# Kernel optimization log

Hardware: AMD Instinct MI355X
Metric: run time of the kernel (lower is better)

## Reference

```python
import jax, jax.numpy as jnp
import numpy as np

N, DEG, D_COORD, D_CH, D_HID = 20000, 32, 3, 64, 256
E = N * DEG


def setup_inputs() -> dict:
    key = jax.random.key(0)
    ks = jax.random.split(key, 12)
    y = jax.random.normal(ks[0], (N, D_COORD), dtype=jnp.float32)
    x = jax.random.normal(ks[1], (N, D_COORD), dtype=jnp.float32)
    f_y = jax.random.normal(ks[2], (N, D_CH), dtype=jnp.float32)
    # quadrature weights ~ 1/|A(x)| scale
    weights = jax.random.uniform(ks[3], (N,), dtype=jnp.float32) / DEG
    neighbors_index = jax.random.randint(ks[4], (E,), 0, N, dtype=jnp.int32)
    neighbors_row_splits = (jnp.arange(N + 1, dtype=jnp.int32) * DEG)
    d_in = 2 * D_COORD + D_CH  # 70: concat(y_nbr, x_self, f_nbr) for 'nonlinear'
    W1 = jax.random.normal(ks[5], (d_in, D_HID), dtype=jnp.float32) / np.sqrt(d_in)
    b1 = jnp.zeros((D_HID,), dtype=jnp.float32)
    W2 = jax.random.normal(ks[6], (D_HID, D_HID), dtype=jnp.float32) / np.sqrt(D_HID)
    b2 = jnp.zeros((D_HID,), dtype=jnp.float32)
    W3 = jax.random.normal(ks[7], (D_HID, D_CH), dtype=jnp.float32) / np.sqrt(D_HID)
    b3 = jnp.zeros((D_CH,), dtype=jnp.float32)
    return {"y": y, "x": x, "f_y": f_y, "weights": weights,
            "neighbors_index": neighbors_index,
            "neighbors_row_splits": neighbors_row_splits,
            "W1": W1, "b1": b1, "W2": W2, "b2": b2, "W3": W3, "b3": b3}


def reference(y, x, f_y, weights, neighbors_index, neighbors_row_splits,
              W1, b1, W2, b2, W3, b3):
    n = y.shape[0]
    e = neighbors_index.shape[0]
    # CSR -> per-edge segment id (equivalent to torch repeat_interleave(num_reps))
    seg = jnp.searchsorted(neighbors_row_splits, jnp.arange(e), side='right') - 1
    rep_features = y[neighbors_index]      # [E, d1] gathered neighbor coords
    self_features = x[seg]                 # [E, d2] repeated query coords
    in_features = f_y[neighbors_index]     # [E, d3] gathered function values
    # transform_type == 'nonlinear': kernel sees (x, y, f(y))
    agg = jnp.concatenate([rep_features, self_features, in_features], axis=-1)
    h = jax.nn.gelu(agg @ W1 + b1, approximate=False)
    h = jax.nn.gelu(h @ W2 + b2, approximate=False)
    k = h @ W3 + b3                        # [E, d3]
    # (d): k(x,y,f(y)) * f(y), then weighted segment-CSR sum
    msg = weights[neighbors_index][:, None] * (k * in_features)
    out = jax.ops.segment_sum(msg, seg, num_segments=n)  # [n, d3]
    return out[None]  # [1, n, d3] (batch of 1)
```

## Files before the change

kernel.cpp:

```cpp
#include <hip/hip_runtime.h>
#include <math.h>
#include <stdint.h>

#define NN   20000
#define DEG  32
#define DIN  70
#define KP   96
#define DH   256
#define DC   64
#define NT   512
#define ET   64
#define NPB  2

typedef _Float16 f16;
typedef _Float16 f16x4 __attribute__((ext_vector_type(4)));
typedef _Float16 f16x8 __attribute__((ext_vector_type(8)));
typedef float    f32x4 __attribute__((ext_vector_type(4)));

#define AGG_P 104
#define YF_P  72

#define W1T_OFF 0
#define W2T_OFF (256*KP)
#define W3T_OFF (256*KP + 256*DH)
#define YF_OFF  (256*KP + 256*DH + DC*DH)

__device__ __forceinline__ float gelu_fast(float v) {
    float u  = v * 0.70710678118654752f;
    float a  = fabsf(u);
    float t  = __builtin_amdgcn_rcpf(fmaf(0.3275911f, a, 1.0f));
    float p  = fmaf(1.061405429f, t, -1.453152027f);
    p = fmaf(p, t, 1.421413741f);
    p = fmaf(p, t, -0.284496736f);
    p = fmaf(p, t, 0.254829592f);
    p = p * t;
    float e  = __expf(-u * u);
    float er = fmaf(-p, e, 1.0f);
    er = copysignf(er, u);
    return 0.5f * v * (1.0f + er);
}

__device__ __forceinline__ f16* h_at(f16* base, int row, int col) {
    uint32_t off = (uint32_t)(row << 9) + ((uint32_t)(col << 1) ^ (uint32_t)((row & 7) << 4));
    return (f16*)((char*)base + off);
}

__global__ void prep_weights(const float* __restrict__ W1,
                             const float* __restrict__ W2,
                             const float* __restrict__ W3,
                             f16* __restrict__ ws)
{
    int t = blockIdx.x * blockDim.x + threadIdx.x;
    if (t < W2T_OFF) {
        int n = t / KP, k = t - n * KP;
        float v;
        if (k < 3)              v = W1[(3 + k) * DH + n];
        else if (k < 8)         v = 0.0f;
        else if (k < 72)        v = W1[(6 + (k - 8)) * DH + n];
        else if (k < 75)        v = W1[(k - 72) * DH + n];
        else                    v = 0.0f;
        ws[t] = (f16)v;
    } else if (t < W3T_OFF) {
        int u = t - W2T_OFF;
        int n = u >> 8, k = u & 255;
        ws[t] = (f16)W2[k * DH + n];
    } else if (t < W3T_OFF + DC * DH) {
        int u = t - W3T_OFF;
        int n = u >> 8, k = u & 255;
        ws[t] = (f16)W3[k * DC + n];
    }
}

__global__ void prep_yf(const float* __restrict__ y,
                        const float* __restrict__ f_y,
                        f16* __restrict__ yf)
{
    int idx = blockIdx.x * blockDim.x + threadIdx.x;
    if (idx >= NN * YF_P) return;
    int n = idx / YF_P, c = idx - n * YF_P;
    float v;
    if (c < DC)          v = f_y[n * DC + c];
    else if (c < DC + 3) v = y[n * 3 + (c - DC)];
    else                 v = 0.0f;
    yf[idx] = (f16)v;
}

__global__ __launch_bounds__(NT, 6)
void it_mfma_kernel(const float* __restrict__ x,
                    const float* __restrict__ wq,
                    const int*   __restrict__ nbr,
                    const float* __restrict__ b1,
                    const float* __restrict__ b2,
                    const float* __restrict__ b3,
                    const f16*  __restrict__ ws,
                    float* __restrict__ out)
{
    const int blk  = blockIdx.x;
    const int t    = threadIdx.x;
    const int lane = t & 63;
    const int w    = t >> 6;
    const int l15  = lane & 15;
    const int lk   = lane >> 4;

    const f16* w1t = ws + W1T_OFF;
    const f16* w2t = ws + W2T_OFF;
    const f16* w3t = ws + W3T_OFF;
    const f16* yf  = ws + YF_OFF;

    __shared__ __align__(16) unsigned char s_u[ET * DH * 2];
    f16 (*s_agg)[AGG_P] = (f16(*)[AGG_P])s_u;
    f16* s_h0 = (f16*)s_u;
    __shared__ int   s_nbr[ET];
    __shared__ float s_wq[ET];
    __shared__ float s_red[4][DC];

    if (t < ET) {
        int n = nbr[blk * ET + t];
        s_nbr[t] = n;
        s_wq[t]  = wq[n];
    }
    __syncthreads();

    {
        const int e    = t >> 3;
        const int part = t & 7;
        const f16* yfr = yf + (size_t)s_nbr[e] * YF_P;
        f16* aggr = &s_agg[e][0];
        #pragma unroll
        for (int j = 0; j < 2; ++j) {
            int ch = part + j * 8;
            if (ch == 0) {
                int node = blk * NPB + (e >> 5);
                f16x8 v = {};
                v[0] = (f16)x[node*3 + 0];
                v[1] = (f16)x[node*3 + 1];
                v[2] = (f16)x[node*3 + 2];
                *(f16x8*)&aggr[0] = v;
            } else if (ch <= 9) {
                *(f16x8*)&aggr[8*ch] = *(const f16x8*)&yfr[8*(ch-1)];
            } else if (ch < 12) {
                *(f16x8*)&aggr[8*ch] = (f16x8){};
            }
        }
    }
    __syncthreads();

    const int n_base = w * 32;

    f32x4 acc[4][2];

    #pragma unroll
    for (int nj = 0; nj < 2; ++nj) {
        float4 bv = *(const float4*)&b1[n_base + nj*16 + lk*4];
        #pragma unroll
        for (int mi = 0; mi < 4; ++mi) acc[mi][nj] = (f32x4){bv.x, bv.y, bv.z, bv.w};
    }
    #pragma unroll
    for (int ks = 0; ks < KP/32; ++ks) {
        const int k0 = ks*32 + lk*8;
        f16x8 a0 = *(const f16x8*)&s_agg[ 0 + l15][k0];
        f16x8 a1 = *(const f16x8*)&s_agg[16 + l15][k0];
        f16x8 a2 = *(const f16x8*)&s_agg[32 + l15][k0];
        f16x8 a3 = *(const f16x8*)&s_agg[48 + l15][k0];
        #pragma unroll
        for (int nj = 0; nj < 2; ++nj) {
            f16x8 b = *(const f16x8*)&w1t[(n_base + nj*16 + l15) * KP + k0];
            acc[0][nj] = __builtin_amdgcn_mfma_f32_16x16x32_f16(b, a0, acc[0][nj], 0, 0, 0);
            acc[1][nj] = __builtin_amdgcn_mfma_f32_16x16x32_f16(b, a1, acc[1][nj], 0, 0, 0);
            acc[2][nj] = __builtin_amdgcn_mfma_f32_16x16x32_f16(b, a2, acc[2][nj], 0, 0, 0);
            acc[3][nj] = __builtin_amdgcn_mfma_f32_16x16x32_f16(b, a3, acc[3][nj], 0, 0, 0);
        }
    }
    __syncthreads();
    #pragma unroll
    for (int mi = 0; mi < 4; ++mi)
        #pragma unroll
        for (int nj = 0; nj < 2; ++nj) {
            int e  = mi*16 + l15;
            int n0 = n_base + nj*16 + lk*4;
            f16x4 hv;
            #pragma unroll
            for (int r = 0; r < 4; ++r) hv[r] = (f16)gelu_fast(acc[mi][nj][r]);
            *(f16x4*)h_at(s_h0, e, n0) = hv;
        }
    __syncthreads();

    #pragma unroll
    for (int nj = 0; nj < 2; ++nj) {
        float4 bv = *(const float4*)&b2[n_base + nj*16 + lk*4];
        #pragma unroll
        for (int mi = 0; mi < 4; ++mi) acc[mi][nj] = (f32x4){bv.x, bv.y, bv.z, bv.w};
    }
    #pragma unroll 2
    for (int ks = 0; ks < DH/32; ++ks) {
        const int k0 = ks*32 + lk*8;
        f16x8 a0 = *(const f16x8*)h_at(s_h0,  0 + l15, k0);
        f16x8 a1 = *(const f16x8*)h_at(s_h0, 16 + l15, k0);
        f16x8 a2 = *(const f16x8*)h_at(s_h0, 32 + l15, k0);
        f16x8 a3 = *(const f16x8*)h_at(s_h0, 48 + l15, k0);
        #pragma unroll
        for (int nj = 0; nj < 2; ++nj) {
            f16x8 b = *(const f16x8*)&w2t[(n_base + nj*16 + l15) * DH + k0];
            acc[0][nj] = __builtin_amdgcn_mfma_f32_16x16x32_f16(b, a0, acc[0][nj], 0, 0, 0);
            acc[1][nj] = __builtin_amdgcn_mfma_f32_16x16x32_f16(b, a1, acc[1][nj], 0, 0, 0);
            acc[2][nj] = __builtin_amdgcn_mfma_f32_16x16x32_f16(b, a2, acc[2][nj], 0, 0, 0);
            acc[3][nj] = __builtin_amdgcn_mfma_f32_16x16x32_f16(b, a3, acc[3][nj], 0, 0, 0);
        }
    }
    __syncthreads();
    #pragma unroll
    for (int mi = 0; mi < 4; ++mi)
        #pragma unroll
        for (int nj = 0; nj < 2; ++nj) {
            int e  = mi*16 + l15;
            int n0 = n_base + nj*16 + lk*4;
            f16x4 hv;
            #pragma unroll
            for (int r = 0; r < 4; ++r) hv[r] = (f16)gelu_fast(acc[mi][nj][r]);
            *(f16x4*)h_at(s_h0, e, n0) = hv;
        }
    __syncthreads();

    {
        const int g       = w & 3;
        const int ch_base = (w >> 2) * 32;
        f32x4 acc3[2];
        #pragma unroll
        for (int nj = 0; nj < 2; ++nj) {
            float4 bv = *(const float4*)&b3[ch_base + nj*16 + lk*4];
            acc3[nj] = (f32x4){bv.x, bv.y, bv.z, bv.w};
        }
        #pragma unroll 2
        for (int ks = 0; ks < DH/32; ++ks) {
            const int k0 = ks*32 + lk*8;
            f16x8 h = *(const f16x8*)h_at(s_h0, g*16 + l15, k0);
            #pragma unroll
            for (int nj = 0; nj < 2; ++nj) {
                f16x8 wf = *(const f16x8*)&w3t[(ch_base + nj*16 + l15) * DH + k0];
                acc3[nj] = __builtin_amdgcn_mfma_f32_16x16x32_f16(wf, h, acc3[nj], 0, 0, 0);
            }
        }
        const int e = g*16 + l15;
        const f16* yfr = yf + (size_t)s_nbr[e] * YF_P;
        const float wqe = s_wq[e];
        #pragma unroll
        for (int nj = 0; nj < 2; ++nj) {
            f16x4 fq = *(const f16x4*)&yfr[ch_base + nj*16 + lk*4];
            f32x4 p;
            #pragma unroll
            for (int r = 0; r < 4; ++r)
                p[r] = wqe * acc3[nj][r] * (float)fq[r];
            #pragma unroll
            for (int m = 1; m <= 8; m <<= 1) {
                #pragma unroll
                for (int r = 0; r < 4; ++r)
                    p[r] += __shfl_xor(p[r], m, 64);
            }
            if (l15 == 0)
                *(f32x4*)&s_red[g][ch_base + nj*16 + lk*4] = p;
        }
    }
    __syncthreads();

    if (t < NPB * DC) {
        int node = t >> 6, c = t & 63;
        out[(blk * NPB + node) * DC + c] = s_red[2*node][c] + s_red[2*node + 1][c];
    }
}

extern "C" void kernel_launch(void* const* d_in, const int* in_sizes, int n_in,
                              void* d_out, int out_size, void* d_ws, size_t ws_size,
                              hipStream_t stream) {
    const float* y   = (const float*)d_in[0];
    const float* x   = (const float*)d_in[1];
    const float* f_y = (const float*)d_in[2];
    const float* wq  = (const float*)d_in[3];
    const int*   nbr = (const int*)d_in[4];
    const float* W1  = (const float*)d_in[6];
    const float* b1  = (const float*)d_in[7];
    const float* W2  = (const float*)d_in[8];
    const float* b2  = (const float*)d_in[9];
    const float* W3  = (const float*)d_in[10];
    const float* b3  = (const float*)d_in[11];
    float* out = (float*)d_out;
    f16*   ws  = (f16*)d_ws;

    hipLaunchKernelGGL(prep_weights, dim3((W3T_OFF + DC*DH + 255) / 256), dim3(256), 0, stream,
                       W1, W2, W3, ws);
    hipLaunchKernelGGL(prep_yf, dim3((NN * YF_P + 255) / 256), dim3(256), 0, stream,
                       y, f_y, ws + YF_OFF);
    hipLaunchKernelGGL(it_mfma_kernel, dim3(NN / NPB), dim3(NT), 0, stream,
                       x, wq, nbr, b1, b2, b3, ws, out);
}
```

Baseline: 375.5 us.

## Split LDS buffers, swizzle h layout, prefetch weights, reuse gathered features

Gives the activation buffer its own LDS region instead of aliasing it with the aggregated-input buffer. Layer-1 output can then be written without the barrier that kept layer-1 reads from overlapping it, and layer-3 reads f(y) from LDS instead of re-gathering it from global memory. Weight fragments are now prefetched one k-step ahead, and LDS addresses use precomputed swizzled offsets. The cost is more LDS per block (about 13 KB extra), which may lower occupancy against the 6-block launch bound. The shared neighbor-index staging is also dropped, so each thread reloads nbr and wq from global memory.

```diff
diff --git a/kernel.cpp b/kernel.cpp
--- a/kernel.cpp
+++ b/kernel.cpp
@@ -4,7 +4,6 @@
 
 #define NN   20000
 #define DEG  32
-#define DIN  70
 #define KP   96
 #define DH   256
 #define DC   64
@@ -38,11 +37,6 @@
     float er = fmaf(-p, e, 1.0f);
     er = copysignf(er, u);
     return 0.5f * v * (1.0f + er);
-}
-
-__device__ __forceinline__ f16* h_at(f16* base, int row, int col) {
-    uint32_t off = (uint32_t)(row << 9) + ((uint32_t)(col << 1) ^ (uint32_t)((row & 7) << 4));
-    return (f16*)((char*)base + off);
 }
 
 __global__ void prep_weights(const float* __restrict__ W1,
@@ -89,9 +83,9 @@
 void it_mfma_kernel(const float* __restrict__ x,
                     const float* __restrict__ wq,
                     const int*   __restrict__ nbr,
-                    const float* __restrict__ b1,
-                    const float* __restrict__ b2,
-                    const float* __restrict__ b3,
+                    const float* __restrict__ bias1,
+                    const float* __restrict__ bias2,
+                    const float* __restrict__ bias3,
                     const f16*  __restrict__ ws,
                     float* __restrict__ out)
 {
@@ -101,30 +95,24 @@
     const int w    = t >> 6;
     const int l15  = lane & 15;
     const int lk   = lane >> 4;
+    const int mm   = l15 & 7;
+    const int mlo  = mm & 3, mhi = mm >> 2;
 
     const f16* w1t = ws + W1T_OFF;
     const f16* w2t = ws + W2T_OFF;
     const f16* w3t = ws + W3T_OFF;
     const f16* yf  = ws + YF_OFF;
 
-    __shared__ __align__(16) unsigned char s_u[ET * DH * 2];
-    f16 (*s_agg)[AGG_P] = (f16(*)[AGG_P])s_u;
-    f16* s_h0 = (f16*)s_u;
-    __shared__ int   s_nbr[ET];
-    __shared__ float s_wq[ET];
+    __shared__ __align__(16) f16 s_agg[ET][AGG_P];
+    __shared__ __align__(16) f16 s_h[ET * DH];
     __shared__ float s_red[4][DC];
-
-    if (t < ET) {
-        int n = nbr[blk * ET + t];
-        s_nbr[t] = n;
-        s_wq[t]  = wq[n];
-    }
-    __syncthreads();
+    f16* s_h0 = s_h;
 
     {
         const int e    = t >> 3;
         const int part = t & 7;
-        const f16* yfr = yf + (size_t)s_nbr[e] * YF_P;
+        const int n    = nbr[blk * ET + e];
+        const f16* yfr = yf + (size_t)n * YF_P;
         f16* aggr = &s_agg[e][0];
         #pragma unroll
         for (int j = 0; j < 2; ++j) {
@@ -147,114 +135,165 @@
 
     const int n_base = w * 32;
 
+    uint32_t rbE[4], rbO[4];
+    #pragma unroll
+    for (int mi = 0; mi < 4; ++mi) {
+        rbE[mi] = (uint32_t)((mi*16 + l15) << 9) + (uint32_t)(mhi << 6)
+                + (uint32_t)((lk ^ mlo) << 4);
+        rbO[mi] = rbE[mi] ^ 64u;
+    }
+    const uint32_t wb = (uint32_t)(l15 << 9) + (uint32_t)((w >> 1) << 7)
+                      + (uint32_t)(((w & 1) ^ mhi) << 6)
+                      + (uint32_t)(((mm >> 1) & 1) << 5)
+                      + (uint32_t)((lk << 3) ^ ((mm & 1) << 4));
+    char* wp0 = (char*)s_h0 + wb;
+    char* wp1 = (char*)s_h0 + (wb ^ 32u);
+
     f32x4 acc[4][2];
+
+    {
+        const f16* w1r0 = &w1t[(n_base + l15) * KP];
+        const f16* w1r1 = &w1t[(n_base + 16 + l15) * KP];
+        f16x8 wf0[3], wf1[3];
+        #pragma unroll
+        for (int ks = 0; ks < 3; ++ks) {
+            wf0[ks] = *(const f16x8*)&w1r0[ks*32 + lk*8];
+            wf1[ks] = *(const f16x8*)&w1r1[ks*32 + lk*8];
+        }
+        #pragma unroll
+        for (int nj = 0; nj < 2; ++nj) {
+            float4 bv = *(const float4*)&bias1[n_base + nj*16 + lk*4];
+            #pragma unroll
+            for (int mi = 0; mi < 4; ++mi) acc[mi][nj] = (f32x4){bv.x, bv.y, bv.z, bv.w};
+        }
+        #pragma unroll
+        for (int ks = 0; ks < 3; ++ks) {
+            f16x8 a0 = *(const f16x8*)&s_agg[ 0 + l15][ks*32 + lk*8];
+            f16x8 a1 = *(const f16x8*)&s_agg[16 + l15][ks*32 + lk*8];
+            f16x8 a2 = *(const f16x8*)&s_agg[32 + l15][ks*32 + lk*8];
+            f16x8 a3 = *(const f16x8*)&s_agg[48 + l15][ks*32 + lk*8];
+            acc[0][0] = __builtin_amdgcn_mfma_f32_16x16x32_f16(wf0[ks], a0, acc[0][0], 0, 0, 0);
+            acc[0][1] = __builtin_amdgcn_mfma_f32_16x16x32_f16(wf1[ks], a0, acc[0][1], 0, 0, 0);
+            acc[1][0] = __builtin_amdgcn_mfma_f32_16x16x32_f16(wf0[ks], a1, acc[1][0], 0, 0, 0);
+            acc[1][1] = __builtin_amdgcn_mfma_f32_16x16x32_f16(wf1[ks], a1, acc[1][1], 0, 0, 0);
+            acc[2][0] = __builtin_amdgcn_mfma_f32_16x16x32_f16(wf0[ks], a2, acc[2][0], 0, 0, 0);
+            acc[2][1] = __builtin_amdgcn_mfma_f32_16x16x32_f16(wf1[ks], a2, acc[2][1], 0, 0, 0);
+            acc[3][0] = __builtin_amdgcn_mfma_f32_16x16x32_f16(wf0[ks], a3, acc[3][0], 0, 0, 0);
+            acc[3][1] = __builtin_amdgcn_mfma_f32_16x16x32_f16(wf1[ks], a3, acc[3][1], 0, 0, 0);
+        }
+    }
+    #pragma unroll
+    for (int mi = 0; mi < 4; ++mi) {
+        #pragma unroll
+        for (int nj = 0; nj < 2; ++nj) {
+            f16x4 hv;
+            #pragma unroll
+            for (int r = 0; r < 4; ++r) hv[r] = (f16)gelu_fast(acc[mi][nj][r]);
+            *(f16x4*)((nj ? wp1 : wp0) + mi*8192) = hv;
+        }
+    }
+    __syncthreads();
 
     #pragma unroll
     for (int nj = 0; nj < 2; ++nj) {
-        float4 bv = *(const float4*)&b1[n_base + nj*16 + lk*4];
+        float4 bv = *(const float4*)&bias2[n_base + nj*16 + lk*4];
         #pragma unroll
         for (int mi = 0; mi < 4; ++mi) acc[mi][nj] = (f32x4){bv.x, bv.y, bv.z, bv.w};
     }
+    {
+        const f16* w2r0 = &w2t[(n_base + l15) * DH];
+        const f16* w2r1 = &w2t[(n_base + 16 + l15) * DH];
+        f16x8 bc0 = *(const f16x8*)&w2r0[lk*8];
+        f16x8 bc1 = *(const f16x8*)&w2r1[lk*8];
+        #pragma unroll
+        for (int ks = 0; ks < 8; ++ks) {
+            f16x8 bn0, bn1;
+            if (ks < 7) {
+                bn0 = *(const f16x8*)&w2r0[(ks+1)*32 + lk*8];
+                bn1 = *(const f16x8*)&w2r1[(ks+1)*32 + lk*8];
+            }
+            const uint32_t ro = (uint32_t)(ks >> 1) * 128u;
+            f16x8 a0, a1, a2, a3;
+            if (ks & 1) {
+                a0 = *(const f16x8*)((char*)s_h0 + rbO[0] + ro);
+                a1 = *(const f16x8*)((char*)s_h0 + rbO[1] + ro);
+                a2 = *(const f16x8*)((char*)s_h0 + rbO[2] + ro);
+                a3 = *(const f16x8*)((char*)s_h0 + rbO[3] + ro);
+            } else {
+                a0 = *(const f16x8*)((char*)s_h0 + rbE[0] + ro);
+                a1 = *(const f16x8*)((char*)s_h0 + rbE[1] + ro);
+                a2 = *(const f16x8*)((char*)s_h0 + rbE[2] + ro);
+                a3 = *(const f16x8*)((char*)s_h0 + rbE[3] + ro);
+            }
+            acc[0][0] = __builtin_amdgcn_mfma_f32_16x16x32_f16(bc0, a0, acc[0][0], 0, 0, 0);
+            acc[0][1] = __builtin_amdgcn_mfma_f32_16x16x32_f16(bc1, a0, acc[0][1], 0, 0, 0);
+            acc[1][0] = __builtin_amdgcn_mfma_f32_16x16x32_f16(bc0, a1, acc[1][0], 0, 0, 0);
+            acc[1][1] = __builtin_amdgcn_mfma_f32_16x16x32_f16(bc1, a1, acc[1][1], 0, 0, 0);
+            acc[2][0] = __builtin_amdgcn_mfma_f32_16x16x32_f16(bc0, a2, acc[2][0], 0, 0, 0);
+            acc[2][1] = __builtin_amdgcn_mfma_f32_16x16x32_f16(bc1, a2, acc[2][1], 0, 0, 0);
+            acc[3][0] = __builtin_amdgcn_mfma_f32_16x16x32_f16(bc0, a3, acc[3][0], 0, 0, 0);
+            acc[3][1] = __builtin_amdgcn_mfma_f32_16x16x32_f16(bc1, a3, acc[3][1], 0, 0, 0);
+            bc0 = bn0; bc1 = bn1;
+        }
+    }
+    __syncthreads();
     #pragma unroll
-    for (int ks = 0; ks < KP/32; ++ks) {
-        const int k0 = ks*32 + lk*8;
-        f16x8 a0 = *(const f16x8*)&s_agg[ 0 + l15][k0];
-        f16x8 a1 = *(const f16x8*)&s_agg[16 + l15][k0];
-        f16x8 a2 = *(const f16x8*)&s_agg[32 + l15][k0];
-        f16x8 a3 = *(const f16x8*)&s_agg[48 + l15][k0];
-        #pragma unroll
-        for (int nj = 0; nj < 2; ++nj) {
-            f16x8 b = *(const f16x8*)&w1t[(n_base + nj*16 + l15) * KP + k0];
-            acc[0][nj] = __builtin_amdgcn_mfma_f32_16x16x32_f16(b, a0, acc[0][nj], 0, 0, 0);
-            acc[1][nj] = __builtin_amdgcn_mfma_f32_16x16x32_f16(b, a1, acc[1][nj], 0, 0, 0);
-            acc[2][nj] = __builtin_amdgcn_mfma_f32_16x16x32_f16(b, a2, acc[2][nj], 0, 0, 0);
-            acc[3][nj] = __builtin_amdgcn_mfma_f32_16x16x32_f16(b, a3, acc[3][nj], 0, 0, 0);
-        }
-    }
-    __syncthreads();
-    #pragma unroll
-    for (int mi = 0; mi < 4; ++mi)
-        #pragma unroll
-        for (int nj = 0; nj < 2; ++nj) {
-            int e  = mi*16 + l15;
-            int n0 = n_base + nj*16 + lk*4;
+    for (int mi = 0; mi < 4; ++mi) {
+        #pragma unroll
+        for (int nj = 0; nj < 2; ++nj) {
             f16x4 hv;
             #pragma unroll
             for (int r = 0; r < 4; ++r) hv[r] = (f16)gelu_fast(acc[mi][nj][r]);
-            *(f16x4*)h_at(s_h0, e, n0) = hv;
-        }
-    __syncthreads();
-
-    #pragma unroll
-    for (int nj = 0; nj < 2; ++nj) {
-        float4 bv = *(const float4*)&b2[n_base + nj*16 + lk*4];
-        #pragma unroll
-        for (int mi = 0; mi < 4; ++mi) acc[mi][nj] = (f32x4){bv.x, bv.y, bv.z, bv.w};
-    }
-    #pragma unroll 2
-    for (int ks = 0; ks < DH/32; ++ks) {
-        const int k0 = ks*32 + lk*8;
-        f16x8 a0 = *(const f16x8*)h_at(s_h0,  0 + l15, k0);
-        f16x8 a1 = *(const f16x8*)h_at(s_h0, 16 + l15, k0);
-        f16x8 a2 = *(const f16x8*)h_at(s_h0, 32 + l15, k0);
-        f16x8 a3 = *(const f16x8*)h_at(s_h0, 48 + l15, k0);
-        #pragma unroll
-        for (int nj = 0; nj < 2; ++nj) {
-            f16x8 b = *(const f16x8*)&w2t[(n_base + nj*16 + l15) * DH + k0];
-            acc[0][nj] = __builtin_amdgcn_mfma_f32_16x16x32_f16(b, a0, acc[0][nj], 0, 0, 0);
-            acc[1][nj] = __builtin_amdgcn_mfma_f32_16x16x32_f16(b, a1, acc[1][nj], 0, 0, 0);
-            acc[2][nj] = __builtin_amdgcn_mfma_f32_16x16x32_f16(b, a2, acc[2][nj], 0, 0, 0);
-            acc[3][nj] = __builtin_amdgcn_mfma_f32_16x16x32_f16(b, a3, acc[3][nj], 0, 0, 0);
-        }
-    }
-    __syncthreads();
-    #pragma unroll
-    for (int mi = 0; mi < 4; ++mi)
-        #pragma unroll
-        for (int nj = 0; nj < 2; ++nj) {
-            int e  = mi*16 + l15;
-            int n0 = n_base + nj*16 + lk*4;
-            f16x4 hv;
-            #pragma unroll
-            for (int r = 0; r < 4; ++r) hv[r] = (f16)gelu_fast(acc[mi][nj][r]);
-            *(f16x4*)h_at(s_h0, e, n0) = hv;
-        }
+            *(f16x4*)((nj ? wp1 : wp0) + mi*8192) = hv;
+        }
+    }
     __syncthreads();
 
     {
         const int g       = w & 3;
         const int ch_base = (w >> 2) * 32;
+        const int e       = g*16 + l15;
+        const int   n_e = nbr[blk * ET + e];
+        const float wqe = wq[n_e];
+        const uint32_t r3E = (uint32_t)(e << 9) + (uint32_t)(mhi << 6)
+                           + (uint32_t)((lk ^ mlo) << 4);
+        const uint32_t r3O = r3E ^ 64u;
+
         f32x4 acc3[2];
         #pragma unroll
         for (int nj = 0; nj < 2; ++nj) {
-            float4 bv = *(const float4*)&b3[ch_base + nj*16 + lk*4];
+            float4 bv = *(const float4*)&bias3[ch_base + nj*16 + lk*4];
             acc3[nj] = (f32x4){bv.x, bv.y, bv.z, bv.w};
         }
-        #pragma unroll 2
-        for (int ks = 0; ks < DH/32; ++ks) {
-            const int k0 = ks*32 + lk*8;
-            f16x8 h = *(const f16x8*)h_at(s_h0, g*16 + l15, k0);
-            #pragma unroll
-            for (int nj = 0; nj < 2; ++nj) {
-                f16x8 wf = *(const f16x8*)&w3t[(ch_base + nj*16 + l15) * DH + k0];
-                acc3[nj] = __builtin_amdgcn_mfma_f32_16x16x32_f16(wf, h, acc3[nj], 0, 0, 0);
-            }
-        }
-        const int e = g*16 + l15;
-        const f16* yfr = yf + (size_t)s_nbr[e] * YF_P;
-        const float wqe = s_wq[e];
-        #pragma unroll
-        for (int nj = 0; nj < 2; ++nj) {
-            f16x4 fq = *(const f16x4*)&yfr[ch_base + nj*16 + lk*4];
+        const f16* w3r0 = &w3t[(ch_base + l15) * DH];
+        const f16* w3r1 = &w3t[(ch_base + 16 + l15) * DH];
+        f16x8 c0 = *(const f16x8*)&w3r0[lk*8];
+        f16x8 c1 = *(const f16x8*)&w3r1[lk*8];
+        #pragma unroll
+        for (int ks = 0; ks < 8; ++ks) {
+            f16x8 nn0, nn1;
+            if (ks < 7) {
+                nn0 = *(const f16x8*)&w3r0[(ks+1)*32 + lk*8];
+                nn1 = *(const f16x8*)&w3r1[(ks+1)*32 + lk*8];
+            }
+            const uint32_t ro = (uint32_t)(ks >> 1) * 128u;
+            f16x8 h = *(const f16x8*)((char*)s_h0 + ((ks & 1) ? r3O : r3E) + ro);
+            acc3[0] = __builtin_amdgcn_mfma_f32_16x16x32_f16(c0, h, acc3[0], 0, 0, 0);
+            acc3[1] = __builtin_amdgcn_mfma_f32_16x16x32_f16(c1, h, acc3[1], 0, 0, 0);
+            c0 = nn0; c1 = nn1;
+        }
+        #pragma unroll
+        for (int nj = 0; nj < 2; ++nj) {
+            f16x4 fq = *(const f16x4*)&s_agg[e][8 + ch_base + nj*16 + lk*4];
             f32x4 p;
             #pragma unroll
             for (int r = 0; r < 4; ++r)
                 p[r] = wqe * acc3[nj][r] * (float)fq[r];
             #pragma unroll
-            for (int m = 1; m <= 8; m <<= 1) {
+            for (int sh = 1; sh <= 8; sh <<= 1) {
                 #pragma unroll
                 for (int r = 0; r < 4; ++r)
-                    p[r] += __shfl_xor(p[r], m, 64);
+                    p[r] += __shfl_xor(p[r], sh, 64);
             }
             if (l15 == 0)
                 *(f32x4*)&s_red[g][ch_base + nj*16 + lk*4] = p;
```

Result: no change. 382.0 us (+1.7%).
